# Optimization experiments

Hardware: AMD Instinct MI355X
Metric: run time of the kernel (lower is better)

The kernel has to match this reference:

```python
import jax, jax.numpy as jnp
import numpy as np

# --- simulation constants (from MPMSimulator.__init__ / builder calls) ---
N_STEPS, N_SUBSTEPS = 20, 30          # 20 frames x 30 substeps = 600 iterations
G = 100                               # grid cells per axis (unit domain)
DX, INV_DX = 0.01, 100.0
DT = 5e-4                             # sim_dt
E, NU = 1.0e5, 0.3
MU = E / (2.0 * (1.0 + NU))
LAM = E * NU / ((1.0 + NU) * (1.0 - 2.0 * NU))
P_VOL = 0.005 ** 3                    # particle spacing 0.005
P_MASS = P_VOL * 3000.0               # density 3000
BOUND = 3                             # sticky boundary thickness (cells)
GRAVITY = np.array([0.0, -9.8, 0.0], np.float32)
_o = np.arange(3)
OFFS = np.stack(np.meshgrid(_o, _o, _o, indexing='ij'), -1).reshape(-1, 3).astype(np.int32)  # (27,3)


def setup_inputs() -> dict:
    key = jax.random.key(0)
    k1, k2 = jax.random.split(key)
    nx, ny, nz, sp = 30, 15, 30, 0.005   # add_mpm_grid dims, jitter=True
    gx = (np.arange(nx) - nx / 2) * sp + 0.5
    gy = np.arange(ny) * sp + 0.2
    gz = (np.arange(nz) - nz / 2) * sp + 0.5
    q = np.stack(np.meshgrid(gx, gy, gz, indexing='ij'), -1).reshape(-1, 3).astype(np.float32)
    jitter = jax.random.uniform(k1, q.shape, jnp.float32, 0.0, 0.5 * sp)
    particle_q = jnp.asarray(q) + jitter
    particle_qd = jnp.zeros_like(particle_q)
    v = jax.random.uniform(k2, (1,), jnp.float32, 0.5e-3, 1.5e-3)  # grid_m_ini value
    return {"v": v, "particle_q": particle_q, "particle_qd": particle_qd}


def _simulate(v, particle_q, particle_qd):
    vscalar = v[0]
    offs = jnp.asarray(OFFS)
    offs_f = offs.astype(jnp.float32)
    grav = jnp.asarray(GRAVITY)
    I3 = jnp.eye(3, dtype=jnp.float32)

    def substep(carry, _):
        x, vel, C, F = carry
        # update deformation gradient, neo-Hookean PK1 stress
        F = jnp.einsum('nij,njk->nik', I3 + DT * C, F)
        J = jnp.linalg.det(F)
        FinvT = jnp.swapaxes(jnp.linalg.inv(F), 1, 2)
        logJ = jnp.log(jnp.maximum(J, 1e-6))
        P = MU * (F - FinvT) + LAM * logJ[:, None, None] * FinvT
        stress = (-DT * P_VOL * 4.0 * INV_DX * INV_DX) * jnp.einsum('nij,nkj->nik', P, F)
        affine = stress + P_MASS * C

        # quadratic B-spline weights over 3x3x3 stencil
        base = jnp.floor(x * INV_DX - 0.5).astype(jnp.int32)          # (N,3)
        fx = x * INV_DX - base.astype(jnp.float32)                    # (N,3)
        w = jnp.stack([0.5 * (1.5 - fx) ** 2,
                       0.75 - (fx - 1.0) ** 2,
                       0.5 * (fx - 0.5) ** 2], 0)                     # (3,N,3)
        weight = (w[offs[:, 0], :, 0] * w[offs[:, 1], :, 1] * w[offs[:, 2], :, 2]).T  # (N,27)
        dpos = (offs_f[None] - fx[:, None, :]) * DX                   # (N,27,3)

        # P2G scatter (gravity folded into momentum, as p2g takes gravity)
        mom = weight[..., None] * (P_MASS * (vel + DT * grav)[:, None, :]
                                   + jnp.einsum('nij,nkj->nki', affine, dpos))  # (N,27,3)
        node = jnp.clip(base[:, None, :] + offs[None], 0, G - 1)
        idx = (node[..., 0] * G + node[..., 1]) * G + node[..., 2]    # (N,27)
        idxf = idx.reshape(-1)
        grid_v = jnp.zeros((G * G * G, 3), jnp.float32).at[idxf].add(mom.reshape(-1, 3))
        grid_m = jnp.zeros((G * G * G,), jnp.float32).at[idxf].add((weight * P_MASS).reshape(-1))

        # grid op: grid mass is initialized to grid_m_ini = v (set_optim_variables)
        gv = grid_v / (grid_m + vscalar)[:, None]
        gv3 = gv.reshape(G, G, G, 3)
        for axis in range(3):  # sticky-ish domain boundary (set_grid_bound)
            sh = [1, 1, 1]; sh[axis] = G
            ii = jnp.arange(G).reshape(sh)
            comp = gv3[..., axis]
            comp = jnp.where((ii < BOUND) & (comp < 0), 0.0, comp)
            comp = jnp.where((ii >= G - BOUND) & (comp > 0), 0.0, comp)
            gv3 = gv3.at[..., axis].set(comp)
        gv = gv3.reshape(-1, 3)

        # G2P gather
        gathered = gv[idx]                                            # (N,27,3)
        new_v = jnp.einsum('nk,nki->ni', weight, gathered)
        new_C = (4.0 * INV_DX * INV_DX) * jnp.einsum('nk,nki,nkj->nij', weight, gathered, dpos)
        return (x + DT * new_v, new_v, new_C, F), grid_m

    substep_ck = jax.checkpoint(substep)

    def frame(carry, _):
        carry, gms = jax.lax.scan(substep_ck, carry, None, length=N_SUBSTEPS)
        # extract_grad_tensor: grid mass of last substep (incl. grid_m_ini offset)
        return carry, gms[-1].reshape(G, G, G) + vscalar

    n = particle_q.shape[0]
    carry0 = (particle_q, particle_qd,
              jnp.zeros((n, 3, 3), jnp.float32),
              jnp.tile(I3, (n, 1, 1)))
    _, grid_m_seq = jax.lax.scan(jax.checkpoint(frame), carry0, None, length=N_STEPS)
    return grid_m_seq  # (N_STEPS, G, G, G)


def reference(v, particle_q, particle_qd):
    return _simulate(v, particle_q, particle_qd)
```

## Files before the change

kernel.cpp:

```cpp
#include <hip/hip_runtime.h>
#include <hip/hip_cooperative_groups.h>

namespace cg = cooperative_groups;

static constexpr int G    = 100;
static constexpr int G3   = G * G * G;
static constexpr int NP   = 13500;
static constexpr int NSUB = 600;
static constexpr int SPF  = 30;
static constexpr int NTHR = 1024;
static constexpr int NBLK = 108;
static constexpr int TCIN  = 2048;
static constexpr int TCOUT = 2048;

__device__ __forceinline__ int clampi(int v) {
    return v < 0 ? 0 : (v > G - 1 ? G - 1 : v);
}

__device__ __forceinline__ void cell_zero(float4* p) {
    unsigned long long* q = reinterpret_cast<unsigned long long*>(p);
    __hip_atomic_store(&q[0], 0ull, __ATOMIC_RELAXED, __HIP_MEMORY_SCOPE_AGENT);
    __hip_atomic_store(&q[1], 0ull, __ATOMIC_RELAXED, __HIP_MEMORY_SCOPE_AGENT);
}

__device__ __forceinline__ void gridbar(unsigned* __restrict__ cnt, unsigned gen) {
    __syncthreads();
    if (threadIdx.x == 0) {
        __hip_atomic_fetch_add(cnt, 1u, __ATOMIC_RELAXED, __HIP_MEMORY_SCOPE_AGENT);
        const unsigned target = gen * (unsigned)NBLK;
        while (__hip_atomic_load(cnt, __ATOMIC_RELAXED, __HIP_MEMORY_SCOPE_AGENT) < target) {
            __builtin_amdgcn_s_sleep(1);
        }
        __builtin_amdgcn_fence(__ATOMIC_ACQUIRE, "agent");
    }
    __syncthreads();
}

__launch_bounds__(NTHR)
__global__ void mpm_sim(const float* __restrict__ vscal,
                        const float* __restrict__ q0,
                        const float* __restrict__ qd0,
                        float* __restrict__ out,
                        float* __restrict__ ws,
                        unsigned* __restrict__ barcnt)
{
    const float vs = vscal[0];
    float4* const g4 = reinterpret_cast<float4*>(ws);

    cg::grid_group gg = cg::this_grid();
    const int tid = blockIdx.x * NTHR + threadIdx.x;
    const int nth = NBLK * NTHR;

    const int slot = threadIdx.x >> 2;
    const int sub  = threadIdx.x & 3;
    const bool act = slot < 125;
    int pid = 0;
    if (act) {
        const int b  = blockIdx.x;
        const int bx = b / 18;
        const int by = (b / 6) % 3;
        const int bz = b % 6;
        const int lx = slot / 25;
        const int rem = slot % 25;
        const int ly = rem / 5;
        const int lz = rem % 5;
        const int ix = bx * 5 + lx;
        const int iy = by * 5 + ly;
        const int iz = bz * 5 + lz;
        pid = (ix * 15 + iy) * 30 + iz;
    }

    const float DT      = 5e-4f;
    const float INV_DX  = 100.0f;
    const float DXc     = 0.01f;
    const float MU      = (float)(1.0e5 / (2.0 * (1.0 + 0.3)));
    const float LAM     = (float)(1.0e5 * 0.3 / ((1.0 + 0.3) * (1.0 - 0.6)));
    const float P_MASS  = (float)(0.005 * 0.005 * 0.005 * 3000.0);
    const float KS      = (float)(-5.0e-4 * (0.005 * 0.005 * 0.005) * 4.0 * 100.0 * 100.0);
    const float DTG     = (float)(5.0e-4 * (-9.8));
    const float CSC     = 4.0f * INV_DX * INV_DX;

    __shared__ float4 tileIn[TCIN];
    __shared__ float  tileOut[4 * TCOUT];
    __shared__ int sred[6];

    {
        const float4 z = make_float4(0.f, 0.f, 0.f, 0.f);
        for (int i = tid; i < 3 * G3; i += nth) g4[i] = z;
        if (tid == 0)
            __hip_atomic_store(barcnt, 0u, __ATOMIC_RELAXED, __HIP_MEMORY_SCOPE_AGENT);
    }

    float px = 0.f, py = 0.f, pz = 0.f, vx = 0.f, vy = 0.f, vz = 0.f;
    float C00 = 0.f, C01 = 0.f, C02 = 0.f,
          C10 = 0.f, C11 = 0.f, C12 = 0.f,
          C20 = 0.f, C21 = 0.f, C22 = 0.f;
    float F00 = 1.f, F01 = 0.f, F02 = 0.f,
          F10 = 0.f, F11 = 1.f, F12 = 0.f,
          F20 = 0.f, F21 = 0.f, F22 = 1.f;
    if (act) {
        px = q0[3 * pid + 0]; py = q0[3 * pid + 1]; pz = q0[3 * pid + 2];
        vx = qd0[3 * pid + 0]; vy = qd0[3 * pid + 1]; vz = qd0[3 * pid + 2];
    }

    int pmn0 = 0, pmn1 = 0, pmn2 = 0, pmx0 = -1, pmx1 = -1, pmx2 = -1; bool pvalid = false;
    int zmn0 = 0, zmn1 = 0, zmn2 = 0, zmx0 = -1, zmx1 = -1, zmx2 = -1; bool zvalid = false;

    gg.sync();

    unsigned gen = 0;

    for (int p = 0; p < NSUB; ++p) {
        const int bS = p % 3;
        const int bG = (p + 2) % 3;
        const int bZ = (p + 1) % 3;
        float4*       __restrict__ gS4 = g4 + bS * G3;
        const float4* __restrict__ gG4 = g4 + bG * G3;
        float4*       __restrict__ gZ4 = g4 + bZ * G3;

        if (zvalid) {
            const int zD1 = zmx1 - zmn1 + 1, zD2 = zmx2 - zmn2 + 1;
            const int zvol = (zmx0 - zmn0 + 1) * zD1 * zD2;
            for (int c = threadIdx.x; c < zvol; c += NTHR) {
                const int k = c % zD2;
                const int t = c / zD2;
                const int j = t % zD1;
                const int i = t / zD1;
                cell_zero(&gZ4[((zmn0 + i) * G + (zmn1 + j)) * G + (zmn2 + k)]);
            }
        }

        if (p > 0 && ((p - 1) % SPF) == SPF - 1) {
            float* o = out + ((p - 1) / SPF) * G3;
            for (int i = tid; i < G3; i += nth) o[i] = gG4[i].w + vs;
        }

        const int iD1 = pvalid ? (pmx1 - pmn1 + 1) : 0;
        const int iD2 = pvalid ? (pmx2 - pmn2 + 1) : 0;
        const int inVol = pvalid ? (pmx0 - pmn0 + 1) * iD1 * iD2 : 0;
        const bool staged = pvalid && (inVol <= TCIN);
        if (staged) {
            for (int c = threadIdx.x; c < inVol; c += NTHR) {
                const int k = c % iD2;
                const int t = c / iD2;
                const int j = t % iD1;
                const int i = t / iD1;
                const int nx = pmn0 + i, ny = pmn1 + j, nz = pmn2 + k;
                const float4 gq = gG4[(nx * G + ny) * G + nz];
                const float den = gq.w + vs;
                float gvx = gq.x / den;
                float gvy = gq.y / den;
                float gvz = gq.z / den;
                if (nx < 3       && gvx < 0.f) gvx = 0.f;
                if (nx >= G - 3  && gvx > 0.f) gvx = 0.f;
                if (ny < 3       && gvy < 0.f) gvy = 0.f;
                if (ny >= G - 3  && gvy > 0.f) gvy = 0.f;
                if (nz < 3       && gvz < 0.f) gvz = 0.f;
                if (nz >= G - 3  && gvz > 0.f) gvz = 0.f;
                tileIn[c] = make_float4(gvx, gvy, gvz, 0.f);
            }
        }
        __syncthreads();

        int sb0 = 0, sb1 = 0, sb2 = 0;
        float fx0 = 0.f, fx1 = 0.f, fx2 = 0.f;
        float A00 = 0.f, A01 = 0.f, A02 = 0.f,
              A10 = 0.f, A11 = 0.f, A12 = 0.f,
              A20 = 0.f, A21 = 0.f, A22 = 0.f;
        float mvx = 0.f, mvy = 0.f, mvz = 0.f;

        if (act) {
            if (p > 0) {
                const float xs0 = px * INV_DX, xs1 = py * INV_DX, xs2 = pz * INV_DX;
                const float fb0 = floorf(xs0 - 0.5f), fb1 = floorf(xs1 - 0.5f), fb2 = floorf(xs2 - 0.5f);
                const int b0 = (int)fb0, b1 = (int)fb1, b2 = (int)fb2;
                const float gx0 = xs0 - fb0, gx1 = xs1 - fb1, gx2 = xs2 - fb2;
                float wa[3], wb[3], wc[3];
                wa[0] = 0.5f * (1.5f - gx0) * (1.5f - gx0);
                wa[1] = 0.75f - (gx0 - 1.0f) * (gx0 - 1.0f);
                wa[2] = 0.5f * (gx0 - 0.5f) * (gx0 - 0.5f);
                wb[0] = 0.5f * (1.5f - gx1) * (1.5f - gx1);
                wb[1] = 0.75f - (gx1 - 1.0f) * (gx1 - 1.0f);
                wb[2] = 0.5f * (gx1 - 0.5f) * (gx1 - 0.5f);
                wc[0] = 0.5f * (1.5f - gx2) * (1.5f - gx2);
                wc[1] = 0.75f - (gx2 - 1.0f) * (gx2 - 1.0f);
                wc[2] = 0.5f * (gx2 - 0.5f) * (gx2 - 0.5f);

                float nvx = 0.f, nvy = 0.f, nvz = 0.f;
                float nc00 = 0.f, nc01 = 0.f, nc02 = 0.f,
                      nc10 = 0.f, nc11 = 0.f, nc12 = 0.f,
                      nc20 = 0.f, nc21 = 0.f, nc22 = 0.f;
                #pragma unroll
                for (int t = 0; t < 7; ++t) {
                    const int c = sub + 4 * t;
                    if (c >= 27) break;
                    const int oi = c / 9;
                    const int rem = c - 9 * oi;
                    const int oj = rem / 3;
                    const int ok = rem - 3 * oj;
                    const int nx = clampi(b0 + oi);
                    const int ny = clampi(b1 + oj);
                    const int nz = clampi(b2 + ok);
                    const float dpx = ((float)oi - gx0) * DXc;
                    const float dpy = ((float)oj - gx1) * DXc;
                    const float dpz = ((float)ok - gx2) * DXc;
                    const float w = wa[oi] * wb[oj] * wc[ok];
                    float gvx, gvy, gvz;
                    if (staged) {
                        const float4 gv4 = tileIn[((nx - pmn0) * iD1 + (ny - pmn1)) * iD2 + (nz - pmn2)];
                        gvx = gv4.x; gvy = gv4.y; gvz = gv4.z;
                    } else {
                        const float4 gq = gG4[(nx * G + ny) * G + nz];
                        const float den = gq.w + vs;
                        gvx = gq.x / den;
                        gvy = gq.y / den;
                        gvz = gq.z / den;
                        if (nx < 3       && gvx < 0.f) gvx = 0.f;
                        if (nx >= G - 3  && gvx > 0.f) gvx = 0.f;
                        if (ny < 3       && gvy < 0.f) gvy = 0.f;
                        if (ny >= G - 3  && gvy > 0.f) gvy = 0.f;
                        if (nz < 3       && gvz < 0.f) gvz = 0.f;
                        if (nz >= G - 3  && gvz > 0.f) gvz = 0.f;
                    }
                    nvx += w * gvx; nvy += w * gvy; nvz += w * gvz;
                    const float wgx = w * gvx, wgy = w * gvy, wgz = w * gvz;
                    nc00 += wgx * dpx; nc01 += wgx * dpy; nc02 += wgx * dpz;
                    nc10 += wgy * dpx; nc11 += wgy * dpy; nc12 += wgy * dpz;
                    nc20 += wgz * dpx; nc21 += wgz * dpy; nc22 += wgz * dpz;
                }
                #define BFLY(v) { v += __shfl_xor(v, 1); v += __shfl_xor(v, 2); }
                BFLY(nvx) BFLY(nvy) BFLY(nvz)
                BFLY(nc00) BFLY(nc01) BFLY(nc02)
                BFLY(nc10) BFLY(nc11) BFLY(nc12)
                BFLY(nc20) BFLY(nc21) BFLY(nc22)
                #undef BFLY
                vx = nvx; vy = nvy; vz = nvz;
                C00 = CSC * nc00; C01 = CSC * nc01; C02 = CSC * nc02;
                C10 = CSC * nc10; C11 = CSC * nc11; C12 = CSC * nc12;
                C20 = CSC * nc20; C21 = CSC * nc21; C22 = CSC * nc22;
                px += DT * vx; py += DT * vy; pz += DT * vz;
            }

            {
                const float t00 = F00 + DT * (C00 * F00 + C01 * F10 + C02 * F20);
                const float t01 = F01 + DT * (C00 * F01 + C01 * F11 + C02 * F21);
                const float t02 = F02 + DT * (C00 * F02 + C01 * F12 + C02 * F22);
                const float t10 = F10 + DT * (C10 * F00 + C11 * F10 + C12 * F20);
                const float t11 = F11 + DT * (C10 * F01 + C11 * F11 + C12 * F21);
                const float t12 = F12 + DT * (C10 * F02 + C11 * F12 + C12 * F22);
                const float t20 = F20 + DT * (C20 * F00 + C21 * F10 + C22 * F20);
                const float t21 = F21 + DT * (C20 * F01 + C21 * F11 + C22 * F21);
                const float t22 = F22 + DT * (C20 * F02 + C21 * F12 + C22 * F22);
                F00 = t00; F01 = t01; F02 = t02;
                F10 = t10; F11 = t11; F12 = t12;
                F20 = t20; F21 = t21; F22 = t22;
            }

            const float c00 = F11 * F22 - F12 * F21;
            const float c01 = F12 * F20 - F10 * F22;
            const float c02 = F10 * F21 - F11 * F20;
            const float det = F00 * c00 + F01 * c01 + F02 * c02;
            const float c10 = F02 * F21 - F01 * F22;
            const float c11 = F00 * F22 - F02 * F20;
            const float c12 = F01 * F20 - F00 * F21;
            const float c20 = F01 * F12 - F02 * F11;
            const float c21 = F02 * F10 - F00 * F12;
            const float c22 = F00 * F11 - F01 * F10;
            const float idet = 1.0f / det;
            const float lj = LAM * logf(fmaxf(det, 1e-6f));
            const float fit00 = c00 * idet, fit01 = c01 * idet, fit02 = c02 * idet;
            const float fit10 = c10 * idet, fit11 = c11 * idet, fit12 = c12 * idet;
            const float fit20 = c20 * idet, fit21 = c21 * idet, fit22 = c22 * idet;
            const float P00 = MU * (F00 - fit00) + lj * fit00;
            const float P01 = MU * (F01 - fit01) + lj * fit01;
            const float P02 = MU * (F02 - fit02) + lj * fit02;
            const float P10 = MU * (F10 - fit10) + lj * fit10;
            const float P11 = MU * (F11 - fit11) + lj * fit11;
            const float P12 = MU * (F12 - fit12) + lj * fit12;
            const float P20 = MU * (F20 - fit20) + lj * fit20;
            const float P21 = MU * (F21 - fit21) + lj * fit21;
            const float P22 = MU * (F22 - fit22) + lj * fit22;
            A00 = KS * (P00 * F00 + P01 * F01 + P02 * F02) + P_MASS * C00;
            A01 = KS * (P00 * F10 + P01 * F11 + P02 * F12) + P_MASS * C01;
            A02 = KS * (P00 * F20 + P01 * F21 + P02 * F22) + P_MASS * C02;
            A10 = KS * (P10 * F00 + P11 * F01 + P12 * F02) + P_MASS * C10;
            A11 = KS * (P10 * F10 + P11 * F11 + P12 * F12) + P_MASS * C11;
            A12 = KS * (P10 * F20 + P11 * F21 + P12 * F22) + P_MASS * C12;
            A20 = KS * (P20 * F00 + P21 * F01 + P22 * F02) + P_MASS * C20;
            A21 = KS * (P20 * F10 + P21 * F11 + P22 * F12) + P_MASS * C21;
            A22 = KS * (P20 * F20 + P21 * F21 + P22 * F22) + P_MASS * C22;

            const float xs0 = px * INV_DX, xs1 = py * INV_DX, xs2 = pz * INV_DX;
            const float fb0 = floorf(xs0 - 0.5f), fb1 = floorf(xs1 - 0.5f), fb2 = floorf(xs2 - 0.5f);
            sb0 = (int)fb0; sb1 = (int)fb1; sb2 = (int)fb2;
            fx0 = xs0 - fb0; fx1 = xs1 - fb1; fx2 = xs2 - fb2;
            mvx = P_MASS * vx;
            mvy = P_MASS * (vy + DTG);
            mvz = P_MASS * vz;
        }

        if (threadIdx.x == 0) {
            sred[0] = INT_MAX; sred[1] = INT_MAX; sred[2] = INT_MAX;
            sred[3] = INT_MIN; sred[4] = INT_MIN; sred[5] = INT_MIN;
        }
        __syncthreads();
        if (act && sub == 0) {
            atomicMin(&sred[0], clampi(sb0)); atomicMax(&sred[3], clampi(sb0 + 2));
            atomicMin(&sred[1], clampi(sb1)); atomicMax(&sred[4], clampi(sb1 + 2));
            atomicMin(&sred[2], clampi(sb2)); atomicMax(&sred[5], clampi(sb2 + 2));
        }
        __syncthreads();
        const int mn0 = sred[0], mn1 = sred[1], mn2 = sred[2];
        const int mx0 = sred[3], mx1 = sred[4], mx2 = sred[5];
        const bool anyAct = (mx0 >= mn0);
        const int D1 = mx1 - mn1 + 1, D2 = mx2 - mn2 + 1;
        const int vol = anyAct ? (mx0 - mn0 + 1) * D1 * D2 : 0;
        const bool useLDS = anyAct && (vol <= TCOUT);
        __syncthreads();

        float wa0 = 0.f, wa1 = 0.f, wa2 = 0.f, wb0 = 0.f, wb1 = 0.f, wb2 = 0.f,
              wcc0 = 0.f, wcc1 = 0.f, wcc2 = 0.f;
        if (act) {
            wa0 = 0.5f * (1.5f - fx0) * (1.5f - fx0);
            wa1 = 0.75f - (fx0 - 1.0f) * (fx0 - 1.0f);
            wa2 = 0.5f * (fx0 - 0.5f) * (fx0 - 0.5f);
            wb0 = 0.5f * (1.5f - fx1) * (1.5f - fx1);
            wb1 = 0.75f - (fx1 - 1.0f) * (fx1 - 1.0f);
            wb2 = 0.5f * (fx1 - 0.5f) * (fx1 - 0.5f);
            wcc0 = 0.5f * (1.5f - fx2) * (1.5f - fx2);
            wcc1 = 0.75f - (fx2 - 1.0f) * (fx2 - 1.0f);
            wcc2 = 0.5f * (fx2 - 0.5f) * (fx2 - 0.5f);
        }
        const float WA[3] = { wa0, wa1, wa2 };
        const float WB[3] = { wb0, wb1, wb2 };
        const float WC[3] = { wcc0, wcc1, wcc2 };

        if (useLDS) {
            float4* t4 = reinterpret_cast<float4*>(tileOut);
            const float4 z = make_float4(0.f, 0.f, 0.f, 0.f);
            for (int i = threadIdx.x; i < vol; i += NTHR) t4[i] = z;
            __syncthreads();
            if (act) {
                #pragma unroll
                for (int t = 0; t < 7; ++t) {
                    const int c = sub + 4 * t;
                    if (c >= 27) break;
                    const int oi = c / 9;
                    const int rem = c - 9 * oi;
                    const int oj = rem / 3;
                    const int ok = rem - 3 * oj;
                    const int li  = clampi(sb0 + oi) - mn0;
                    const int lj2 = clampi(sb1 + oj) - mn1;
                    const int lk  = clampi(sb2 + ok) - mn2;
                    const float dpx = ((float)oi - fx0) * DXc;
                    const float dpy = ((float)oj - fx1) * DXc;
                    const float dpz = ((float)ok - fx2) * DXc;
                    const float w = WA[oi] * WB[oj] * WC[ok];
                    const int c4 = 4 * ((li * D1 + lj2) * D2 + lk);
                    atomicAdd(&tileOut[c4 + 0], w * (mvx + A00 * dpx + A01 * dpy + A02 * dpz));
                    atomicAdd(&tileOut[c4 + 1], w * (mvy + A10 * dpx + A11 * dpy + A12 * dpz));
                    atomicAdd(&tileOut[c4 + 2], w * (mvz + A20 * dpx + A21 * dpy + A22 * dpz));
                    atomicAdd(&tileOut[c4 + 3], w * P_MASS);
                }
            }
            __syncthreads();
            for (int c = threadIdx.x; c < vol; c += NTHR) {
                const float m = tileOut[4 * c + 3];
                if (m != 0.f) {
                    const int k = c % D2;
                    const int t = c / D2;
                    const int j = t % D1;
                    const int i = t / D1;
                    const int gidx = ((mn0 + i) * G + (mn1 + j)) * G + (mn2 + k);
                    float* gp = reinterpret_cast<float*>(gS4 + gidx);
                    unsafeAtomicAdd(gp + 0, tileOut[4 * c + 0]);
                    unsafeAtomicAdd(gp + 1, tileOut[4 * c + 1]);
                    unsafeAtomicAdd(gp + 2, tileOut[4 * c + 2]);
                    unsafeAtomicAdd(gp + 3, m);
                }
            }
        } else if (anyAct && act) {
            #pragma unroll
            for (int t = 0; t < 7; ++t) {
                const int c = sub + 4 * t;
                if (c >= 27) break;
                const int oi = c / 9;
                const int rem = c - 9 * oi;
                const int oj = rem / 3;
                const int ok = rem - 3 * oj;
                const int nx = clampi(sb0 + oi);
                const int ny = clampi(sb1 + oj);
                const int nz = clampi(sb2 + ok);
                const float dpx = ((float)oi - fx0) * DXc;
                const float dpy = ((float)oj - fx1) * DXc;
                const float dpz = ((float)ok - fx2) * DXc;
                const float w = WA[oi] * WB[oj] * WC[ok];
                float* gp = reinterpret_cast<float*>(gS4 + (nx * G + ny) * G + nz);
                unsafeAtomicAdd(gp + 0, w * (mvx + A00 * dpx + A01 * dpy + A02 * dpz));
                unsafeAtomicAdd(gp + 1, w * (mvy + A10 * dpx + A11 * dpy + A12 * dpz));
                unsafeAtomicAdd(gp + 2, w * (mvz + A20 * dpx + A21 * dpy + A22 * dpz));
                unsafeAtomicAdd(gp + 3, w * P_MASS);
            }
        }

        zmn0 = pmn0; zmn1 = pmn1; zmn2 = pmn2;
        zmx0 = pmx0; zmx1 = pmx1; zmx2 = pmx2; zvalid = pvalid;
        pmn0 = mn0; pmn1 = mn1; pmn2 = mn2;
        pmx0 = mx0; pmx1 = mx1; pmx2 = mx2; pvalid = anyAct;

        gridbar(barcnt, ++gen);
    }

    {
        const float4* gL4 = g4 + ((NSUB - 1) % 3) * G3;
        float* o = out + (NSUB / SPF - 1) * G3;
        for (int i = tid; i < G3; i += nth) o[i] = gL4[i].w + vs;
    }
}

extern "C" void kernel_launch(void* const* d_in, const int* in_sizes, int n_in,
                              void* d_out, int out_size, void* d_ws, size_t ws_size,
                              hipStream_t stream) {
    const float* v  = (const float*)d_in[0];
    const float* q  = (const float*)d_in[1];
    const float* qd = (const float*)d_in[2];
    float* out = (float*)d_out;
    float* ws  = (float*)d_ws;
    unsigned* barcnt = reinterpret_cast<unsigned*>((char*)d_ws + (ws_size & ~(size_t)15) - 16);
    void* args[] = { (void*)&v, (void*)&q, (void*)&qd, (void*)&out, (void*)&ws, (void*)&barcnt };
    hipLaunchCooperativeKernel(reinterpret_cast<void*>(mpm_sim),
                               dim3(NBLK), dim3(NTHR), args, 0, stream);
}
```

Baseline: 19.07 ms.

## Spread output init across substeps and scatter frame mass directly into output

Instead of copying the full grid mass into the output after each frame, the kernel now fills each frame's output with the offset value in chunks across the first 29 substeps. During the last substep of the frame it atomically adds the P2G mass contributions straight into the output. The block size is halved and tile zeroing plus bound-reduction setup move earlier to remove some block barriers. The acquire fence in the grid barrier is dropped, and grid reads use relaxed atomic loads instead. Dropping the fence risks memory-ordering bugs, and the per-frame work now adds atomics into the output.

```diff
diff --git a/kernel.cpp b/kernel.cpp
--- a/kernel.cpp
+++ b/kernel.cpp
@@ -8,15 +8,27 @@
 static constexpr int NP   = 13500;
 static constexpr int NSUB = 600;
 static constexpr int SPF  = 30;
-static constexpr int NTHR = 1024;
+static constexpr int NTHR = 512;
 static constexpr int NBLK = 108;
 static constexpr int TCIN  = 2048;
 static constexpr int TCOUT = 2048;
+static constexpr int CH   = (G3 + SPF - 2) / (SPF - 1);
 
 __device__ __forceinline__ int clampi(int v) {
     return v < 0 ? 0 : (v > G - 1 ? G - 1 : v);
 }
 
+__device__ __forceinline__ float4 cell_load(const float4* p) {
+    const unsigned long long* q = reinterpret_cast<const unsigned long long*>(p);
+    unsigned long long a = __hip_atomic_load(&q[0], __ATOMIC_RELAXED, __HIP_MEMORY_SCOPE_AGENT);
+    unsigned long long b = __hip_atomic_load(&q[1], __ATOMIC_RELAXED, __HIP_MEMORY_SCOPE_AGENT);
+    float4 r;
+    r.x = __uint_as_float((unsigned)(a & 0xffffffffu));
+    r.y = __uint_as_float((unsigned)(a >> 32));
+    r.z = __uint_as_float((unsigned)(b & 0xffffffffu));
+    r.w = __uint_as_float((unsigned)(b >> 32));
+    return r;
+}
 __device__ __forceinline__ void cell_zero(float4* p) {
     unsigned long long* q = reinterpret_cast<unsigned long long*>(p);
     __hip_atomic_store(&q[0], 0ull, __ATOMIC_RELAXED, __HIP_MEMORY_SCOPE_AGENT);
@@ -31,7 +43,6 @@
         while (__hip_atomic_load(cnt, __ATOMIC_RELAXED, __HIP_MEMORY_SCOPE_AGENT) < target) {
             __builtin_amdgcn_s_sleep(1);
         }
-        __builtin_amdgcn_fence(__ATOMIC_ACQUIRE, "agent");
     }
     __syncthreads();
 }
@@ -117,7 +128,25 @@
         float4*       __restrict__ gS4 = g4 + bS * G3;
         const float4* __restrict__ gG4 = g4 + bG * G3;
         float4*       __restrict__ gZ4 = g4 + bZ * G3;
-
+        const int fc = p % SPF;
+        float* const outF = (fc == SPF - 1) ? (out + (p / SPF) * G3) : nullptr;
+
+        if (threadIdx.x == 0) {
+            sred[0] = INT_MAX; sred[1] = INT_MAX; sred[2] = INT_MAX;
+            sred[3] = INT_MIN; sred[4] = INT_MIN; sred[5] = INT_MIN;
+        }
+        if (fc < SPF - 1) {
+            float* of = out + (p / SPF) * G3;
+            const int beg = fc * CH;
+            const int end = (beg + CH < G3) ? beg + CH : G3;
+            for (int i = beg + tid; i < end; i += nth)
+                __hip_atomic_store(&of[i], vs, __ATOMIC_RELAXED, __HIP_MEMORY_SCOPE_AGENT);
+        }
+        {
+            float4* t4 = reinterpret_cast<float4*>(tileOut);
+            const float4 z = make_float4(0.f, 0.f, 0.f, 0.f);
+            for (int i = threadIdx.x; i < TCOUT; i += NTHR) t4[i] = z;
+        }
         if (zvalid) {
             const int zD1 = zmx1 - zmn1 + 1, zD2 = zmx2 - zmn2 + 1;
             const int zvol = (zmx0 - zmn0 + 1) * zD1 * zD2;
@@ -129,12 +158,6 @@
                 cell_zero(&gZ4[((zmn0 + i) * G + (zmn1 + j)) * G + (zmn2 + k)]);
             }
         }
-
-        if (p > 0 && ((p - 1) % SPF) == SPF - 1) {
-            float* o = out + ((p - 1) / SPF) * G3;
-            for (int i = tid; i < G3; i += nth) o[i] = gG4[i].w + vs;
-        }
-
         const int iD1 = pvalid ? (pmx1 - pmn1 + 1) : 0;
         const int iD2 = pvalid ? (pmx2 - pmn2 + 1) : 0;
         const int inVol = pvalid ? (pmx0 - pmn0 + 1) * iD1 * iD2 : 0;
@@ -146,7 +169,7 @@
                 const int j = t % iD1;
                 const int i = t / iD1;
                 const int nx = pmn0 + i, ny = pmn1 + j, nz = pmn2 + k;
-                const float4 gq = gG4[(nx * G + ny) * G + nz];
+                const float4 gq = cell_load(&gG4[(nx * G + ny) * G + nz]);
                 const float den = gq.w + vs;
                 float gvx = gq.x / den;
                 float gvy = gq.y / den;
@@ -210,7 +233,7 @@
                         const float4 gv4 = tileIn[((nx - pmn0) * iD1 + (ny - pmn1)) * iD2 + (nz - pmn2)];
                         gvx = gv4.x; gvy = gv4.y; gvz = gv4.z;
                     } else {
-                        const float4 gq = gG4[(nx * G + ny) * G + nz];
+                        const float4 gq = cell_load(&gG4[(nx * G + ny) * G + nz]);
                         const float den = gq.w + vs;
                         gvx = gq.x / den;
                         gvy = gq.y / den;
@@ -297,26 +320,21 @@
             mvx = P_MASS * vx;
             mvy = P_MASS * (vy + DTG);
             mvz = P_MASS * vz;
-        }
-
-        if (threadIdx.x == 0) {
-            sred[0] = INT_MAX; sred[1] = INT_MAX; sred[2] = INT_MAX;
-            sred[3] = INT_MIN; sred[4] = INT_MIN; sred[5] = INT_MIN;
+
+            if (sub == 0) {
+                atomicMin(&sred[0], clampi(sb0)); atomicMax(&sred[3], clampi(sb0 + 2));
+                atomicMin(&sred[1], clampi(sb1)); atomicMax(&sred[4], clampi(sb1 + 2));
+                atomicMin(&sred[2], clampi(sb2)); atomicMax(&sred[5], clampi(sb2 + 2));
+            }
         }
         __syncthreads();
-        if (act && sub == 0) {
-            atomicMin(&sred[0], clampi(sb0)); atomicMax(&sred[3], clampi(sb0 + 2));
-            atomicMin(&sred[1], clampi(sb1)); atomicMax(&sred[4], clampi(sb1 + 2));
-            atomicMin(&sred[2], clampi(sb2)); atomicMax(&sred[5], clampi(sb2 + 2));
-        }
-        __syncthreads();
+
         const int mn0 = sred[0], mn1 = sred[1], mn2 = sred[2];
         const int mx0 = sred[3], mx1 = sred[4], mx2 = sred[5];
         const bool anyAct = (mx0 >= mn0);
         const int D1 = mx1 - mn1 + 1, D2 = mx2 - mn2 + 1;
         const int vol = anyAct ? (mx0 - mn0 + 1) * D1 * D2 : 0;
         const bool useLDS = anyAct && (vol <= TCOUT);
-        __syncthreads();
 
         float wa0 = 0.f, wa1 = 0.f, wa2 = 0.f, wb0 = 0.f, wb1 = 0.f, wb2 = 0.f,
               wcc0 = 0.f, wcc1 = 0.f, wcc2 = 0.f;
@@ -336,10 +354,6 @@
         const float WC[3] = { wcc0, wcc1, wcc2 };
 
         if (useLDS) {
-            float4* t4 = reinterpret_cast<float4*>(tileOut);
-            const float4 z = make_float4(0.f, 0.f, 0.f, 0.f);
-            for (int i = threadIdx.x; i < vol; i += NTHR) t4[i] = z;
-            __syncthreads();
             if (act) {
                 #pragma unroll
                 for (int t = 0; t < 7; ++t) {
@@ -377,30 +391,36 @@
                     unsafeAtomicAdd(gp + 1, tileOut[4 * c + 1]);
                     unsafeAtomicAdd(gp + 2, tileOut[4 * c + 2]);
                     unsafeAtomicAdd(gp + 3, m);
+                    if (outF) unsafeAtomicAdd(&outF[gidx], m);
                 }
             }
-        } else if (anyAct && act) {
-            #pragma unroll
-            for (int t = 0; t < 7; ++t) {
-                const int c = sub + 4 * t;
-                if (c >= 27) break;
-                const int oi = c / 9;
-                const int rem = c - 9 * oi;
-                const int oj = rem / 3;
-                const int ok = rem - 3 * oj;
-                const int nx = clampi(sb0 + oi);
-                const int ny = clampi(sb1 + oj);
-                const int nz = clampi(sb2 + ok);
-                const float dpx = ((float)oi - fx0) * DXc;
-                const float dpy = ((float)oj - fx1) * DXc;
-                const float dpz = ((float)ok - fx2) * DXc;
-                const float w = WA[oi] * WB[oj] * WC[ok];
-                float* gp = reinterpret_cast<float*>(gS4 + (nx * G + ny) * G + nz);
-                unsafeAtomicAdd(gp + 0, w * (mvx + A00 * dpx + A01 * dpy + A02 * dpz));
-                unsafeAtomicAdd(gp + 1, w * (mvy + A10 * dpx + A11 * dpy + A12 * dpz));
-                unsafeAtomicAdd(gp + 2, w * (mvz + A20 * dpx + A21 * dpy + A22 * dpz));
-                unsafeAtomicAdd(gp + 3, w * P_MASS);
-            }
+        } else {
+            if (anyAct && act) {
+                #pragma unroll
+                for (int t = 0; t < 7; ++t) {
+                    const int c = sub + 4 * t;
+                    if (c >= 27) break;
+                    const int oi = c / 9;
+                    const int rem = c - 9 * oi;
+                    const int oj = rem / 3;
+                    const int ok = rem - 3 * oj;
+                    const int nx = clampi(sb0 + oi);
+                    const int ny = clampi(sb1 + oj);
+                    const int nz = clampi(sb2 + ok);
+                    const float dpx = ((float)oi - fx0) * DXc;
+                    const float dpy = ((float)oj - fx1) * DXc;
+                    const float dpz = ((float)ok - fx2) * DXc;
+                    const float w = WA[oi] * WB[oj] * WC[ok];
+                    const int gidx = (nx * G + ny) * G + nz;
+                    float* gp = reinterpret_cast<float*>(gS4 + gidx);
+                    unsafeAtomicAdd(gp + 0, w * (mvx + A00 * dpx + A01 * dpy + A02 * dpz));
+                    unsafeAtomicAdd(gp + 1, w * (mvy + A10 * dpx + A11 * dpy + A12 * dpz));
+                    unsafeAtomicAdd(gp + 2, w * (mvz + A20 * dpx + A21 * dpy + A22 * dpz));
+                    unsafeAtomicAdd(gp + 3, w * P_MASS);
+                    if (outF) unsafeAtomicAdd(&outF[gidx], w * P_MASS);
+                }
+            }
+            __syncthreads();
         }
 
         zmn0 = pmn0; zmn1 = pmn1; zmn2 = pmn2;
@@ -408,13 +428,7 @@
         pmn0 = mn0; pmn1 = mn1; pmn2 = mn2;
         pmx0 = mx0; pmx1 = mx1; pmx2 = mx2; pvalid = anyAct;
 
-        gridbar(barcnt, ++gen);
-    }
-
-    {
-        const float4* gL4 = g4 + ((NSUB - 1) % 3) * G3;
-        float* o = out + (NSUB / SPF - 1) * G3;
-        for (int i = tid; i < G3; i += nth) o[i] = gL4[i].w + vs;
+        if (p < NSUB - 1) gridbar(barcnt, ++gen);
     }
 }
 
```

Measured after the change: 18.16 ms. -4.8%, faster.
